# Performance work log

Measured on AMD Instinct MI355X. Metric: run time of the kernel, lower is better.

Reference implementation:

```python
import jax, jax.numpy as jnp
import numpy as np

NUM_STUDENTS = 50000
NUM_PROBLEMS = 10000
EMBED_DIM = 64
NNZ = 3200000


def _spmm(rows, cols, vals, x, num_out):
    # out[r] = sum_{edges e with rows[e]==r} vals[e] * x[cols[e]]
    msgs = vals[:, None] * x[cols]  # [nnz, d]
    return jax.ops.segment_sum(msgs, rows, num_segments=num_out)


def setup_inputs() -> dict:
    key = jax.random.key(0)
    ks = jax.random.split(key, 8)
    return {
        "student_embeds": jax.random.normal(ks[0], (NUM_STUDENTS, EMBED_DIM), jnp.float32),
        "problem_embeds": jax.random.normal(ks[1], (NUM_PROBLEMS, EMBED_DIM), jnp.float32),
        "a_rows": jax.random.randint(ks[2], (NNZ,), 0, NUM_STUDENTS, jnp.int32),
        "a_cols": jax.random.randint(ks[3], (NNZ,), 0, NUM_PROBLEMS, jnp.int32),
        "a_vals": jax.random.uniform(ks[4], (NNZ,), jnp.float32),
        "ia_rows": jax.random.randint(ks[5], (NNZ,), 0, NUM_STUDENTS, jnp.int32),
        "ia_cols": jax.random.randint(ks[6], (NNZ,), 0, NUM_PROBLEMS, jnp.int32),
        "ia_vals": jax.random.uniform(ks[7], (NNZ,), jnp.float32),
    }


def reference(student_embeds, problem_embeds, a_rows, a_cols, a_vals,
              ia_rows, ia_cols, ia_vals):
    num_students = student_embeds.shape[0]
    num_problems = problem_embeds.shape[0]
    # a_matrix @ problem_embeds
    student_embeds_c = _spmm(a_rows, a_cols, a_vals, problem_embeds, num_students)
    # a_matrix.T @ student_embeds (swap roles of rows/cols)
    problem_embeds_c = _spmm(a_cols, a_rows, a_vals, student_embeds, num_problems)
    student_embeds_ic = _spmm(ia_rows, ia_cols, ia_vals, problem_embeds, num_students)
    problem_embeds_ic = _spmm(ia_cols, ia_rows, ia_vals, student_embeds, num_problems)
    return (student_embeds_c, student_embeds_ic, problem_embeds_c, problem_embeds_ic)
```

## Files before the change

kernel.cpp:

```cpp
#include <hip/hip_runtime.h>
#include <hip/hip_bf16.h>

#define NBMAX 256
#define TILE  4096
#define KPT   16
#define FTILE 2048
#define FKPT  8
#define BINSMAX 512

__device__ __forceinline__ int seg8(unsigned r, unsigned mult8) {
    return (int)__umulhi(r, mult8);
}

__global__ __launch_bounds__(256) void hist_all(
        const int* __restrict__ k0, const int* __restrict__ k1,
        const int* __restrict__ k2, const int* __restrict__ k3,
        int* __restrict__ gcnt4, int nnz, int rsh_s, int rsh_p) {
    __shared__ int h[NBMAX];
    int dir = blockIdx.x & 3;
    const int* key = (dir == 0) ? k0 : (dir == 1) ? k1 : (dir == 2) ? k2 : k3;
    int rsh = (dir & 1) ? rsh_p : rsh_s;
    h[threadIdx.x] = 0;
    __syncthreads();
    int ch = blockIdx.x >> 2, nch = gridDim.x >> 2;
    int nnz4 = nnz >> 2;
    for (int i = ch * 256 + threadIdx.x; i < nnz4; i += nch * 256) {
        int4 k4 = ((const int4*)key)[i];
        atomicAdd(&h[k4.x >> rsh], 1);
        atomicAdd(&h[k4.y >> rsh], 1);
        atomicAdd(&h[k4.z >> rsh], 1);
        atomicAdd(&h[k4.w >> rsh], 1);
    }
    if (ch == 0) {
        for (int i = (nnz4 << 2) + threadIdx.x; i < nnz; i += 256)
            atomicAdd(&h[key[i] >> rsh], 1);
    }
    __syncthreads();
    int v = h[threadIdx.x];
    if (v) atomicAdd(&gcnt4[dir * NBMAX + threadIdx.x], v);
}

__global__ __launch_bounds__(256) void scan_all(
        const int* __restrict__ gcnt4, int* __restrict__ boffs4,
        int* __restrict__ bcur4, int nb_s, int nb_p, int nnz,
        int* __restrict__ offsE, int* __restrict__ offsO, int NS, int NP8) {
    __shared__ int tmp[NBMAX];
    int dir = blockIdx.x, tid = threadIdx.x;
    int nb = (dir & 1) ? nb_p : nb_s;
    int v = (tid < nb) ? gcnt4[dir * NBMAX + tid] : 0;
    tmp[tid] = v;
    __syncthreads();
    for (int off = 1; off < NBMAX; off <<= 1) {
        int t = (tid >= off) ? tmp[tid - off] : 0;
        __syncthreads();
        tmp[tid] += t;
        __syncthreads();
    }
    if (tid < nb) {
        int e = tmp[tid] - v;
        boffs4[dir * (NBMAX + 1) + tid] = e;
        bcur4[dir * NBMAX + tid] = e;
    }
    if (tid == 0) boffs4[dir * (NBMAX + 1) + nb] = nnz;
    if (dir == 0 && tid == 0) { offsE[NS] = nnz; offsO[NP8] = nnz; }
}

__global__ __launch_bounds__(256) void staged_scatter(
        const int* __restrict__ key, const int* __restrict__ other,
        const float* __restrict__ vals, int* __restrict__ cursor,
        uint2* __restrict__ edges, int nnz, int rsh) {
    __shared__ int lhist[NBMAX], lofs[NBMAX], lbase[NBMAX];
    __shared__ uint2 stage[TILE];
    __shared__ int   sslot[TILE];
    int tid = threadIdx.x;
    int lmask = (1 << rsh) - 1;
    int ntiles = (nnz + TILE - 1) / TILE;
    for (int tile = blockIdx.x; tile < ntiles; tile += gridDim.x) {
        int tbeg = tile * TILE;
        int n = nnz - tbeg; if (n > TILE) n = TILE;
        lhist[tid] = 0;
        __syncthreads();
        int myb[KPT], myr[KPT]; unsigned myo[KPT]; float myv[KPT];
        #pragma unroll
        for (int g = 0; g < 4; ++g) {
            int s = g * 1024 + tid * 4;
            if (s + 4 <= n) {
                int i = tbeg + s;
                int4   k4 = *(const int4*)(key + i);
                int4   o4 = *(const int4*)(other + i);
                float4 v4 = *(const float4*)(vals + i);
                int   kk[4] = {k4.x, k4.y, k4.z, k4.w};
                int   oo[4] = {o4.x, o4.y, o4.z, o4.w};
                float vv[4] = {v4.x, v4.y, v4.z, v4.w};
                #pragma unroll
                for (int k = 0; k < 4; ++k) {
                    int m = g * 4 + k;
                    myb[m] = kk[k] >> rsh;
                    myo[m] = (unsigned)oo[k] | ((unsigned)(kk[k] & lmask) << 16);
                    myv[m] = vv[k];
                    myr[m] = atomicAdd(&lhist[myb[m]], 1);
                }
            } else {
                #pragma unroll
                for (int k = 0; k < 4; ++k) {
                    int m = g * 4 + k;
                    int s2 = s + k;
                    if (s2 < n) {
                        int i = tbeg + s2;
                        int ky = key[i];
                        myb[m] = ky >> rsh;
                        myo[m] = (unsigned)other[i] | ((unsigned)(ky & lmask) << 16);
                        myv[m] = vals[i];
                        myr[m] = atomicAdd(&lhist[myb[m]], 1);
                    } else myb[m] = -1;
                }
            }
        }
        __syncthreads();
        int h = lhist[tid];
        lofs[tid] = h;
        __syncthreads();
        for (int off = 1; off < NBMAX; off <<= 1) {
            int t = (tid >= off) ? lofs[tid - off] : 0;
            __syncthreads();
            lofs[tid] += t;
            __syncthreads();
        }
        lofs[tid] -= h;
        if (h > 0) lbase[tid] = atomicAdd(&cursor[tid], h);
        __syncthreads();
        #pragma unroll
        for (int k = 0; k < KPT; ++k) {
            if (myb[k] >= 0) {
                int ls = lofs[myb[k]] + myr[k];
                stage[ls] = make_uint2(myo[k], __float_as_uint(myv[k]));
                sslot[ls] = lbase[myb[k]] + myr[k];
            }
        }
        __syncthreads();
        #pragma unroll
        for (int k = 0; k < KPT; ++k) {
            int s = k * 256 + tid;
            if (s < n) edges[sslot[s]] = stage[s];
        }
        __syncthreads();
    }
}

__global__ __launch_bounds__(256) void staged_scatter2(
        const int* __restrict__ krow, const int* __restrict__ kcol,
        const float* __restrict__ vals,
        int* __restrict__ curE, int* __restrict__ curO,
        uint2* __restrict__ edgesE, uint2* __restrict__ edgesO,
        int nnz, int rsh_e, int rsh_o) {
    __shared__ int lhistE[NBMAX], lofsE[NBMAX], lbaseE[NBMAX];
    __shared__ int lhistO[NBMAX], lofsO[NBMAX], lbaseO[NBMAX];
    __shared__ uint2 stageE[FTILE], stageO[FTILE];
    __shared__ int   sslotE[FTILE], sslotO[FTILE];
    int tid = threadIdx.x;
    int lmE = (1 << rsh_e) - 1, lmO = (1 << rsh_o) - 1;
    int ntiles = (nnz + FTILE - 1) / FTILE;
    for (int tile = blockIdx.x; tile < ntiles; tile += gridDim.x) {
        int tbeg = tile * FTILE;
        int n = nnz - tbeg; if (n > FTILE) n = FTILE;
        lhistE[tid] = 0; lhistO[tid] = 0;
        __syncthreads();
        int mbE[FKPT], mrE[FKPT]; unsigned moE[FKPT];
        int mbO[FKPT], mrO[FKPT]; unsigned moO[FKPT];
        float mv[FKPT];
        #pragma unroll
        for (int g = 0; g < 2; ++g) {
            int s = g * 1024 + tid * 4;
            if (s + 4 <= n) {
                int i = tbeg + s;
                int4   r4 = *(const int4*)(krow + i);
                int4   c4 = *(const int4*)(kcol + i);
                float4 v4 = *(const float4*)(vals + i);
                int   rr[4] = {r4.x, r4.y, r4.z, r4.w};
                int   cc[4] = {c4.x, c4.y, c4.z, c4.w};
                float vv[4] = {v4.x, v4.y, v4.z, v4.w};
                #pragma unroll
                for (int k = 0; k < 4; ++k) {
                    int m = g * 4 + k;
                    mv[m]  = vv[k];
                    mbE[m] = rr[k] >> rsh_e;
                    moE[m] = (unsigned)cc[k] | ((unsigned)(rr[k] & lmE) << 16);
                    mrE[m] = atomicAdd(&lhistE[mbE[m]], 1);
                    mbO[m] = cc[k] >> rsh_o;
                    moO[m] = (unsigned)rr[k] | ((unsigned)(cc[k] & lmO) << 16);
                    mrO[m] = atomicAdd(&lhistO[mbO[m]], 1);
                }
            } else {
                #pragma unroll
                for (int k = 0; k < 4; ++k) {
                    int m = g * 4 + k;
                    int s2 = s + k;
                    if (s2 < n) {
                        int i = tbeg + s2;
                        int r = krow[i], c = kcol[i];
                        mv[m]  = vals[i];
                        mbE[m] = r >> rsh_e;
                        moE[m] = (unsigned)c | ((unsigned)(r & lmE) << 16);
                        mrE[m] = atomicAdd(&lhistE[mbE[m]], 1);
                        mbO[m] = c >> rsh_o;
                        moO[m] = (unsigned)r | ((unsigned)(c & lmO) << 16);
                        mrO[m] = atomicAdd(&lhistO[mbO[m]], 1);
                    } else { mbE[m] = -1; mbO[m] = -1; }
                }
            }
        }
        __syncthreads();
        int hE = lhistE[tid], hO = lhistO[tid];
        lofsE[tid] = hE; lofsO[tid] = hO;
        __syncthreads();
        for (int off = 1; off < NBMAX; off <<= 1) {
            int tE = (tid >= off) ? lofsE[tid - off] : 0;
            int tO = (tid >= off) ? lofsO[tid - off] : 0;
            __syncthreads();
            lofsE[tid] += tE; lofsO[tid] += tO;
            __syncthreads();
        }
        lofsE[tid] -= hE; lofsO[tid] -= hO;
        if (hE > 0) lbaseE[tid] = atomicAdd(&curE[tid], hE);
        if (hO > 0) lbaseO[tid] = atomicAdd(&curO[tid], hO);
        __syncthreads();
        #pragma unroll
        for (int k = 0; k < FKPT; ++k) {
            if (mbE[k] >= 0) {
                int lsE = lofsE[mbE[k]] + mrE[k];
                stageE[lsE] = make_uint2(moE[k], __float_as_uint(mv[k]));
                sslotE[lsE] = lbaseE[mbE[k]] + mrE[k];
                int lsO = lofsO[mbO[k]] + mrO[k];
                stageO[lsO] = make_uint2(moO[k], __float_as_uint(mv[k]));
                sslotO[lsO] = lbaseO[mbO[k]] + mrO[k];
            }
        }
        __syncthreads();
        #pragma unroll
        for (int k = 0; k < FKPT; ++k) {
            int s = k * 256 + tid;
            if (s < n) {
                edgesE[sslotE[s]] = stageE[s];
                edgesO[sslotO[s]] = stageO[s];
            }
        }
        __syncthreads();
    }
}

__global__ __launch_bounds__(512) void row_sort1(
        const uint2* __restrict__ e1, uint2* __restrict__ e2,
        const int* __restrict__ boffs, int* __restrict__ offs,
        int odd, int nb, int rsh, int nrows, unsigned mult8) {
    __shared__ int cnt[BINSMAX];
    __shared__ int tot[512];
    int tid = threadIdx.x;
    int b = blockIdx.x;
    if (b >= nb) return;
    int bins = odd ? (8 << rsh) : (1 << rsh);
    int beg = boffs[b], end = boffs[b + 1];
    if (tid < bins) cnt[tid] = 0;
    __syncthreads();
    for (int i = beg + tid; i < end; i += 512) {
        uint2 e = e1[i];
        int lrow = (int)(e.x >> 16);
        int bin = odd ? (lrow * 8 + seg8(e.x & 0xFFFFu, mult8)) : lrow;
        atomicAdd(&cnt[bin], 1);
    }
    __syncthreads();
    int own = (tid < bins) ? cnt[tid] : 0;
    tot[tid] = own;
    __syncthreads();
    for (int off = 1; off < 512; off <<= 1) {
        int t = (tid >= off) ? tot[tid - off] : 0;
        __syncthreads();
        tot[tid] += t;
        __syncthreads();
    }
    if (tid < bins) {
        int fineoff = tot[tid] - own;
        cnt[tid] = beg + fineoff;
        if (!odd) {
            int row = (b << rsh) + tid;
            if (row < nrows) offs[row] = beg + fineoff;
        } else {
            int row = (b << rsh) + (tid >> 3);
            if (row < nrows) offs[(row << 3) + (tid & 7)] = beg + fineoff;
        }
    }
    __syncthreads();
    for (int i = beg + tid; i < end; i += 512) {
        uint2 e = e1[i];
        int lrow = (int)(e.x >> 16);
        int bin = odd ? (lrow * 8 + seg8(e.x & 0xFFFFu, mult8)) : lrow;
        int slot = atomicAdd(&cnt[bin], 1);
        e2[slot] = make_uint2(e.x & 0xFFFFu, e.y);
    }
}

__device__ __forceinline__ void chunk_accum(
        float4& acc, uint2 e, int n, const float* __restrict__ xq, int q) {
    int   c0 = __shfl((int)e.x, q);
    float v0 = __uint_as_float(__shfl((int)e.y, q));
    int   c1 = __shfl((int)e.x, 4 + q);
    float v1 = __uint_as_float(__shfl((int)e.y, 4 + q));
    float4 x0 = *(const float4*)(xq + (((size_t)c0) << 6));
    float4 x1 = *(const float4*)(xq + (((size_t)c1) << 6));
    for (int j = 8; j < n; j += 8) {
        int   nc0 = __shfl((int)e.x, j + q);
        float nv0 = __uint_as_float(__shfl((int)e.y, j + q));
        int   nc1 = __shfl((int)e.x, j + 4 + q);
        float nv1 = __uint_as_float(__shfl((int)e.y, j + 4 + q));
        float4 nx0 = *(const float4*)(xq + (((size_t)nc0) << 6));
        float4 nx1 = *(const float4*)(xq + (((size_t)nc1) << 6));
        acc.x += v0 * x0.x; acc.y += v0 * x0.y;
        acc.z += v0 * x0.z; acc.w += v0 * x0.w;
        acc.x += v1 * x1.x; acc.y += v1 * x1.y;
        acc.z += v1 * x1.z; acc.w += v1 * x1.w;
        v0 = nv0; v1 = nv1; x0 = nx0; x1 = nx1;
    }
    acc.x += v0 * x0.x; acc.y += v0 * x0.y;
    acc.z += v0 * x0.z; acc.w += v0 * x0.w;
    acc.x += v1 * x1.x; acc.y += v1 * x1.y;
    acc.z += v1 * x1.z; acc.w += v1 * x1.w;
}

__device__ __forceinline__ float4 gather_pre(
        uint2 e0, int beg, int end, const uint2* __restrict__ edges,
        const float* __restrict__ xq, int q, int lane) {
    float4 acc = make_float4(0.f, 0.f, 0.f, 0.f);
    int n0 = end - beg; if (n0 > 64) n0 = 64;
    chunk_accum(acc, e0, n0, xq, q);
    for (int base = beg + 64; base < end; base += 64) {
        int n = end - base; if (n > 64) n = 64;
        uint2 e = make_uint2(0u, 0u);
        if (lane < n) e = edges[base + lane];
        chunk_accum(acc, e, n, xq, q);
    }
    acc.x += __shfl_xor(acc.x, 16); acc.y += __shfl_xor(acc.y, 16);
    acc.z += __shfl_xor(acc.z, 16); acc.w += __shfl_xor(acc.w, 16);
    acc.x += __shfl_xor(acc.x, 32); acc.y += __shfl_xor(acc.y, 32);
    acc.z += __shfl_xor(acc.z, 32); acc.w += __shfl_xor(acc.w, 32);
    return acc;
}

__global__ __launch_bounds__(256) void row_gather(
        const int* __restrict__ offs, const uint2* __restrict__ edges,
        const float* __restrict__ x, float* __restrict__ out, int nrows) {
    int wave = threadIdx.x >> 6, lane = threadIdx.x & 63;
    int q = lane >> 4, l16 = lane & 15;
    const float* xq = x + (l16 << 2);
    int rA = blockIdx.x * 8 + wave * 2;
    if (rA >= nrows) return;
    int rB = rA + 1;
    int begA = offs[rA], endA = offs[rA + 1];
    int begB = 0, endB = 0;
    if (rB < nrows) { begB = offs[rB]; endB = offs[rB + 1]; }
    int nA = endA - begA; if (nA > 64) nA = 64;
    int nB = endB - begB; if (nB > 64) nB = 64;
    uint2 eA = make_uint2(0u, 0u), eB = make_uint2(0u, 0u);
    if (lane < nA) eA = edges[begA + lane];
    if (lane < nB) eB = edges[begB + lane];
    float4 accA = gather_pre(eA, begA, endA, edges, xq, q, lane);
    if ((lane >> 4) == 0)
        *(float4*)(out + (((size_t)rA) << 6) + (l16 << 2)) = accA;
    if (rB < nrows) {
        float4 accB = gather_pre(eB, begB, endB, edges, xq, q, lane);
        if ((lane >> 4) == 0)
            *(float4*)(out + (((size_t)rB) << 6) + (l16 << 2)) = accB;
    }
}

__global__ __launch_bounds__(256) void xcd_gather(
        const int* __restrict__ offs, const uint2* __restrict__ edges,
        const float* __restrict__ x, float* __restrict__ partial, int NP) {
    int g = blockIdx.x;
    int slot = g & 7;
    int t = g >> 3;
    int wave = threadIdx.x >> 6, lane = threadIdx.x & 63;
    int q = lane >> 4, l16 = lane & 15;
    const float* xq = x + (l16 << 2);
    int rA = t * 8 + wave * 2;
    if (rA >= NP) return;
    int rB = rA + 1;
    int binA = rA * 8 + slot;
    int begA = offs[binA], endA = offs[binA + 1];
    int begB = 0, endB = 0;
    if (rB < NP) { int binB = rB * 8 + slot; begB = offs[binB]; endB = offs[binB + 1]; }
    int nA = endA - begA; if (nA > 64) nA = 64;
    int nB = endB - begB; if (nB > 64) nB = 64;
    uint2 eA = make_uint2(0u, 0u), eB = make_uint2(0u, 0u);
    if (lane < nA) eA = edges[begA + lane];
    if (lane < nB) eB = edges[begB + lane];
    float4 accA = gather_pre(eA, begA, endA, edges, xq, q, lane);
    if ((lane >> 4) == 0)
        *(float4*)(partial + (size_t)slot * NP * 64 + (((size_t)rA) << 6) + (l16 << 2)) = accA;
    if (rB < NP) {
        float4 accB = gather_pre(eB, begB, endB, edges, xq, q, lane);
        if ((lane >> 4) == 0)
            *(float4*)(partial + (size_t)slot * NP * 64 + (((size_t)rB) << 6) + (l16 << 2)) = accB;
    }
}

__global__ __launch_bounds__(256) void reduce8(
        const float* __restrict__ partial, float* __restrict__ out, int n4) {
    int i = blockIdx.x * 256 + threadIdx.x;
    if (i < n4) {
        const float4* p = (const float4*)partial;
        float4 s = make_float4(0.f, 0.f, 0.f, 0.f);
        #pragma unroll
        for (int xx = 0; xx < 8; ++xx) {
            float4 v = p[(size_t)xx * n4 + i];
            s.x += v.x; s.y += v.y; s.z += v.z; s.w += v.w;
        }
        ((float4*)out)[i] = s;
    }
}

__global__ void spmm_scatter_kernel(const int* __restrict__ rows, const int* __restrict__ cols,
                                    const float* __restrict__ vals,
                                    const float* __restrict__ s_emb, const float* __restrict__ p_emb,
                                    float* __restrict__ out_s, float* __restrict__ out_p, int nnz) {
    long long t = (long long)blockIdx.x * blockDim.x + threadIdx.x;
    int e = (int)(t >> 6);
    int d = (int)(t & 63);
    if (e >= nnz) return;
    int r = rows[e];
    int c = cols[e];
    float v = vals[e];
    atomicAdd(&out_s[(size_t)r * 64 + d], v * p_emb[(size_t)c * 64 + d]);
    atomicAdd(&out_p[(size_t)c * 64 + d], v * s_emb[(size_t)r * 64 + d]);
}

extern "C" void kernel_launch(void* const* d_in, const int* in_sizes, int n_in,
                              void* d_out, int out_size, void* d_ws, size_t ws_size,
                              hipStream_t stream) {
    const float* s_emb   = (const float*)d_in[0];
    const float* p_emb   = (const float*)d_in[1];
    const int*   a_rows  = (const int*)d_in[2];
    const int*   a_cols  = (const int*)d_in[3];
    const float* a_vals  = (const float*)d_in[4];
    const int*   ia_rows = (const int*)d_in[5];
    const int*   ia_cols = (const int*)d_in[6];
    const float* ia_vals = (const float*)d_in[7];

    const int NS  = in_sizes[0] / 64;
    const int NP  = in_sizes[1] / 64;
    const int nnz = in_sizes[2];
    const int NP8 = NP * 8;

    float* out = (float*)d_out;
    float* out_sc  = out;
    float* out_sic = out_sc  + (size_t)NS * 64;
    float* out_pc  = out_sic + (size_t)NS * 64;
    float* out_pic = out_pc  + (size_t)NP * 64;

    int rsh_s = 0; while ((((long long)NS + (1LL << rsh_s) - 1) >> rsh_s) > NBMAX) rsh_s++;
    int rsh_p = 0; while ((((long long)NP + (1LL << rsh_p) - 1) >> rsh_p) > NBMAX) rsh_p++;
    int nb_s = (NS + (1 << rsh_s) - 1) >> rsh_s;
    int nb_p = (NP + (1 << rsh_p) - 1) >> rsh_p;
    unsigned mult8 = (unsigned)((8ULL << 32) / (unsigned)NS);

    const size_t edges_bytes = (size_t)nnz * sizeof(uint2);
    const size_t offsE_bytes = (size_t)(NS + 1) * sizeof(int);
    const size_t offsO_bytes = (size_t)(NP8 + 1) * sizeof(int);
    const size_t fixed_bytes = offsE_bytes + offsO_bytes
                      + (size_t)(4 * NBMAX + 4 * (NBMAX + 1) + 4 * NBMAX) * sizeof(int) + 256;
    const size_t need  = 2 * edges_bytes + fixed_bytes;
    const size_t need3 = 3 * edges_bytes + fixed_bytes;
    const bool packable = (NS <= 0xFFFF) && (NP <= 0xFFFF) &&
                          ((1 << rsh_s) <= BINSMAX) && ((8 << rsh_p) <= BINSMAX) &&
                          (edges_bytes >= (size_t)NP8 * 64 * sizeof(float)) &&
                          ((NP * 64) % 4 == 0);

    if (ws_size < need || !packable) {
        hipMemsetAsync(d_out, 0, (size_t)out_size * sizeof(float), stream);
        const long long total = (long long)nnz * 64;
        const int grid = (int)((total + 255) / 256);
        spmm_scatter_kernel<<<grid, 256, 0, stream>>>(a_rows, a_cols, a_vals, s_emb, p_emb,
                                                      out_sc, out_pc, nnz);
        spmm_scatter_kernel<<<grid, 256, 0, stream>>>(ia_rows, ia_cols, ia_vals, s_emb, p_emb,
                                                      out_sic, out_pic, nnz);
        return;
    }

    const bool fused = (ws_size >= need3);

    char* w = (char*)d_ws;
    uint2* edges1 = (uint2*)w;  w += edges_bytes;
    uint2* edges2 = (uint2*)w;  w += edges_bytes;
    uint2* edges3 = nullptr;
    if (fused) { edges3 = (uint2*)w; w += edges_bytes; }
    int*   offsE  = (int*)w;    w += offsE_bytes;
    int*   offsO  = (int*)w;    w += offsO_bytes;
    int*   gcnt4  = (int*)w;    w += 4 * NBMAX * sizeof(int);
    int*   boffs4 = (int*)w;    w += 4 * (NBMAX + 1) * sizeof(int);
    int*   bcur4  = (int*)w;

    hipMemsetAsync(gcnt4, 0, 4 * NBMAX * sizeof(int), stream);
    hist_all<<<1024, 256, 0, stream>>>(a_rows, a_cols, ia_rows, ia_cols,
                                       gcnt4, nnz, rsh_s, rsh_p);
    scan_all<<<4, 256, 0, stream>>>(gcnt4, boffs4, bcur4, nb_s, nb_p, nnz,
                                    offsE, offsO, NS, NP8);

    if (fused) {
        const int ntiles2 = (nnz + FTILE - 1) / FTILE;
        struct Mat { const int* r; const int* c; const float* v;
                     float* oe; float* oo; int de, dodd; };
        Mat mats[2] = {
            { a_rows,  a_cols,  a_vals,  out_sc,  out_pc,  0, 1 },
            { ia_rows, ia_cols, ia_vals, out_sic, out_pic, 2, 3 },
        };
        for (int m = 0; m < 2; ++m) {
            const Mat& M = mats[m];
            staged_scatter2<<<ntiles2, 256, 0, stream>>>(M.r, M.c, M.v,
                    bcur4 + M.de * NBMAX, bcur4 + M.dodd * NBMAX,
                    edges1, edges3, nnz, rsh_s, rsh_p);
            row_sort1<<<nb_s, 512, 0, stream>>>(edges1, edges2,
                    boffs4 + M.de * (NBMAX + 1), offsE, 0, nb_s, rsh_s, NS, mult8);
            row_gather<<<(NS + 7) / 8, 256, 0, stream>>>(offsE, edges2, p_emb, M.oe, NS);
            row_sort1<<<nb_p, 512, 0, stream>>>(edges3, edges1,
                    boffs4 + M.dodd * (NBMAX + 1), offsO, 1, nb_p, rsh_p, NP, mult8);
            xcd_gather<<<8 * ((NP + 7) / 8), 256, 0, stream>>>(offsO, edges1,
                    s_emb, (float*)edges3, NP);
            reduce8<<<(NP * 64 / 4 + 255) / 256, 256, 0, stream>>>((float*)edges3,
                    M.oo, NP * 64 / 4);
        }
        return;
    }

    float* partial = (float*)edges1;
    const int ntiles = (nnz + TILE - 1) / TILE;
    struct Dir { const int* key; const int* other; const float* vals;
                 float* out; int odd; };
    Dir dirs[4] = {
        { a_rows,  a_cols,  a_vals,  out_sc,  0 },
        { a_cols,  a_rows,  a_vals,  out_pc,  1 },
        { ia_rows, ia_cols, ia_vals, out_sic, 0 },
        { ia_cols, ia_rows, ia_vals, out_pic, 1 },
    };
    for (int t = 0; t < 4; ++t) {
        const Dir& D = dirs[t];
        if (!D.odd) {
            staged_scatter<<<ntiles, 256, 0, stream>>>(D.key, D.other, D.vals,
                                                       bcur4 + t * NBMAX, edges1, nnz, rsh_s);
            row_sort1<<<nb_s, 512, 0, stream>>>(edges1, edges2,
                                                boffs4 + t * (NBMAX + 1), offsE,
                                                0, nb_s, rsh_s, NS, mult8);
            row_gather<<<(NS + 7) / 8, 256, 0, stream>>>(offsE, edges2, p_emb, D.out, NS);
        } else {
            staged_scatter<<<ntiles, 256, 0, stream>>>(D.key, D.other, D.vals,
                                                       bcur4 + t * NBMAX, edges1, nnz, rsh_p);
            row_sort1<<<nb_p, 512, 0, stream>>>(edges1, edges2,
                                                boffs4 + t * (NBMAX + 1), offsO,
                                                1, nb_p, rsh_p, NP, mult8);
            xcd_gather<<<8 * ((NP + 7) / 8), 256, 0, stream>>>(offsO, edges2,
                                                               s_emb, partial, NP);
            reduce8<<<(NP * 64 / 4 + 255) / 256, 256, 0, stream>>>(partial, D.out, NP * 64 / 4);
        }
    }
}
```

Measured before the change: 558.0 us.

## Merge independent stages into shared launches to cut kernel count and fill the GPU

Fuses the row-gather of the even direction with the odd-direction fine sort into a single launch, with blocks split by index. The first matrix's 8-way partial reduction is also folded into the second matrix's scatter kernel as extra blocks. The xcd partials move to the edges2 buffer so this works. The aim is to cut launch and tail overhead and let independent work overlap on the CUs. In exchange the mixed kernels run at 512 threads with large shared-memory footprints, which may lower occupancy for the gather part.

```diff
diff --git a/kernel.cpp b/kernel.cpp
--- a/kernel.cpp
+++ b/kernel.cpp
@@ -152,15 +152,32 @@
         const float* __restrict__ vals,
         int* __restrict__ curE, int* __restrict__ curO,
         uint2* __restrict__ edgesE, uint2* __restrict__ edgesO,
-        int nnz, int rsh_e, int rsh_o) {
+        int nnz, int rsh_e, int rsh_o, int sgrid,
+        const float* __restrict__ rpart, float* __restrict__ rout, int n4red) {
     __shared__ int lhistE[NBMAX], lofsE[NBMAX], lbaseE[NBMAX];
     __shared__ int lhistO[NBMAX], lofsO[NBMAX], lbaseO[NBMAX];
     __shared__ uint2 stageE[FTILE], stageO[FTILE];
     __shared__ int   sslotE[FTILE], sslotO[FTILE];
     int tid = threadIdx.x;
+    int nred = (n4red + 255) >> 8;
+    if ((int)blockIdx.x < nred) {
+        int i = blockIdx.x * 256 + tid;
+        if (i < n4red) {
+            const float4* p = (const float4*)rpart;
+            float4 s = make_float4(0.f, 0.f, 0.f, 0.f);
+            #pragma unroll
+            for (int xx = 0; xx < 8; ++xx) {
+                float4 v = p[(size_t)xx * n4red + i];
+                s.x += v.x; s.y += v.y; s.z += v.z; s.w += v.w;
+            }
+            ((float4*)rout)[i] = s;
+        }
+        return;
+    }
+    int sb = blockIdx.x - nred;
     int lmE = (1 << rsh_e) - 1, lmO = (1 << rsh_o) - 1;
     int ntiles = (nnz + FTILE - 1) / FTILE;
-    for (int tile = blockIdx.x; tile < ntiles; tile += gridDim.x) {
+    for (int tile = sb; tile < ntiles; tile += sgrid) {
         int tbeg = tile * FTILE;
         int n = nnz - tbeg; if (n > FTILE) n = FTILE;
         lhistE[tid] = 0; lhistO[tid] = 0;
@@ -344,13 +361,12 @@
     return acc;
 }
 
-__global__ __launch_bounds__(256) void row_gather(
-        const int* __restrict__ offs, const uint2* __restrict__ edges,
-        const float* __restrict__ x, float* __restrict__ out, int nrows) {
-    int wave = threadIdx.x >> 6, lane = threadIdx.x & 63;
+__device__ __forceinline__ void gatherE_body(
+        int rA, const int* __restrict__ offs, const uint2* __restrict__ edges,
+        const float* __restrict__ x, float* __restrict__ out, int nrows,
+        int lane) {
     int q = lane >> 4, l16 = lane & 15;
     const float* xq = x + (l16 << 2);
-    int rA = blockIdx.x * 8 + wave * 2;
     if (rA >= nrows) return;
     int rB = rA + 1;
     int begA = offs[rA], endA = offs[rA + 1];
@@ -368,6 +384,65 @@
         float4 accB = gather_pre(eB, begB, endB, edges, xq, q, lane);
         if ((lane >> 4) == 0)
             *(float4*)(out + (((size_t)rB) << 6) + (l16 << 2)) = accB;
+    }
+}
+
+__global__ __launch_bounds__(256) void row_gather(
+        const int* __restrict__ offs, const uint2* __restrict__ edges,
+        const float* __restrict__ x, float* __restrict__ out, int nrows) {
+    int wave = threadIdx.x >> 6, lane = threadIdx.x & 63;
+    gatherE_body(blockIdx.x * 8 + wave * 2, offs, edges, x, out, nrows, lane);
+}
+
+__global__ __launch_bounds__(512) void gatherE_sortO(
+        const int* __restrict__ offsE_, const uint2* __restrict__ e2g,
+        const float* __restrict__ xg, float* __restrict__ outg, int nrows,
+        const uint2* __restrict__ e1s, uint2* __restrict__ e2s,
+        const int* __restrict__ boffsS, int* __restrict__ offsS,
+        int nb, int rsh, int nrowsS, unsigned mult8) {
+    int tid = threadIdx.x;
+    if ((int)blockIdx.x >= nb) {
+        int gb = blockIdx.x - nb;
+        int wave = tid >> 6, lane = tid & 63;
+        gatherE_body(gb * 16 + wave * 2, offsE_, e2g, xg, outg, nrows, lane);
+        return;
+    }
+    __shared__ int cnt[BINSMAX];
+    __shared__ int tot[512];
+    int b = blockIdx.x;
+    int bins = 8 << rsh;
+    int beg = boffsS[b], end = boffsS[b + 1];
+    if (tid < bins) cnt[tid] = 0;
+    __syncthreads();
+    for (int i = beg + tid; i < end; i += 512) {
+        uint2 e = e1s[i];
+        int lrow = (int)(e.x >> 16);
+        int bin = lrow * 8 + seg8(e.x & 0xFFFFu, mult8);
+        atomicAdd(&cnt[bin], 1);
+    }
+    __syncthreads();
+    int own = (tid < bins) ? cnt[tid] : 0;
+    tot[tid] = own;
+    __syncthreads();
+    for (int off = 1; off < 512; off <<= 1) {
+        int t = (tid >= off) ? tot[tid - off] : 0;
+        __syncthreads();
+        tot[tid] += t;
+        __syncthreads();
+    }
+    if (tid < bins) {
+        int fineoff = tot[tid] - own;
+        cnt[tid] = beg + fineoff;
+        int row = (b << rsh) + (tid >> 3);
+        if (row < nrowsS) offsS[(row << 3) + (tid & 7)] = beg + fineoff;
+    }
+    __syncthreads();
+    for (int i = beg + tid; i < end; i += 512) {
+        uint2 e = e1s[i];
+        int lrow = (int)(e.x >> 16);
+        int bin = lrow * 8 + seg8(e.x & 0xFFFFu, mult8);
+        int slot = atomicAdd(&cnt[bin], 1);
+        e2s[slot] = make_uint2(e.x & 0xFFFFu, e.y);
     }
 }
 
@@ -505,6 +580,9 @@
 
     if (fused) {
         const int ntiles2 = (nnz + FTILE - 1) / FTILE;
+        const int ggrid = (NS + 15) / 16;
+        const int n4red = NP * 64 / 4;
+        const int nred  = (n4red + 255) / 256;
         struct Mat { const int* r; const int* c; const float* v;
                      float* oe; float* oo; int de, dodd; };
         Mat mats[2] = {
@@ -513,19 +591,24 @@
         };
         for (int m = 0; m < 2; ++m) {
             const Mat& M = mats[m];
-            staged_scatter2<<<ntiles2, 256, 0, stream>>>(M.r, M.c, M.v,
+            int red_n4 = (m == 1) ? n4red : 0;
+            int red_blocks = (m == 1) ? nred : 0;
+            staged_scatter2<<<ntiles2 + red_blocks, 256, 0, stream>>>(
+                    M.r, M.c, M.v,
                     bcur4 + M.de * NBMAX, bcur4 + M.dodd * NBMAX,
-                    edges1, edges3, nnz, rsh_s, rsh_p);
+                    edges1, edges3, nnz, rsh_s, rsh_p, ntiles2,
+                    (const float*)edges2, mats[0].oo, red_n4);
             row_sort1<<<nb_s, 512, 0, stream>>>(edges1, edges2,
                     boffs4 + M.de * (NBMAX + 1), offsE, 0, nb_s, rsh_s, NS, mult8);
-            row_gather<<<(NS + 7) / 8, 256, 0, stream>>>(offsE, edges2, p_emb, M.oe, NS);
-            row_sort1<<<nb_p, 512, 0, stream>>>(edges3, edges1,
-                    boffs4 + M.dodd * (NBMAX + 1), offsO, 1, nb_p, rsh_p, NP, mult8);
+            gatherE_sortO<<<nb_p + ggrid, 512, 0, stream>>>(
+                    offsE, edges2, p_emb, M.oe, NS,
+                    edges3, edges1, boffs4 + M.dodd * (NBMAX + 1), offsO,
+                    nb_p, rsh_p, NP, mult8);
             xcd_gather<<<8 * ((NP + 7) / 8), 256, 0, stream>>>(offsO, edges1,
-                    s_emb, (float*)edges3, NP);
-            reduce8<<<(NP * 64 / 4 + 255) / 256, 256, 0, stream>>>((float*)edges3,
-                    M.oo, NP * 64 / 4);
-        }
+                    s_emb, (float*)edges2, NP);
+        }
+        reduce8<<<(n4red + 255) / 256, 256, 0, stream>>>((const float*)edges2,
+                mats[1].oo, n4red);
         return;
     }
 
```

Measured after the change: 536.9 us. 1.04x faster.
